# Performance work log

Measured on AMD Instinct MI355X. Metric: run time of the kernel, lower is better.

## Reference

```python
import jax, jax.numpy as jnp
import numpy as np

HIDDEN = 1024
HEADS = 16
HEAD_DIM = HIDDEN // HEADS  # 64
MAX_SEQ = 2048


def _rope_tables():
    # RotaryEmbedding buffers: freqs_cos/sin of shape [max_seq_len, head_dim//2]
    inv_freq = 1.0 / (10000.0 ** (jnp.arange(0, HEAD_DIM, 2, dtype=jnp.float32) / HEAD_DIM))
    t = jnp.arange(MAX_SEQ, dtype=jnp.float32)
    freqs = t[:, None] * inv_freq[None, :]
    return jnp.cos(freqs), jnp.sin(freqs)


def setup_inputs() -> dict:
    key = jax.random.key(0)
    k1, k2, k3 = jax.random.split(key, 3)
    x = jax.random.normal(k1, (2, 2048, HIDDEN), dtype=jnp.float32)
    qkv_w = jax.random.normal(k2, (HIDDEN, 3 * HIDDEN), dtype=jnp.float32) * 0.02
    qkv_b = jnp.zeros((3 * HIDDEN,), dtype=jnp.float32)
    out_w = jax.random.normal(k3, (HIDDEN, HIDDEN), dtype=jnp.float32) * 0.02
    out_b = jnp.zeros((HIDDEN,), dtype=jnp.float32)
    return {"x": x, "qkv_w": qkv_w, "qkv_b": qkv_b, "out_w": out_w, "out_b": out_b}


def reference(x, qkv_w, qkv_b, out_w, out_b):
    b, s, _ = x.shape
    qkv = x @ qkv_w + qkv_b                                   # [b, s, 3*hidden]
    qkv = qkv.reshape(b, s, HEADS, 3 * HEAD_DIM).transpose(0, 2, 1, 3)  # [b, h, s, 3*hd]
    q, k, v = jnp.split(qkv, 3, axis=-1)                      # each [b, h, s, hd]

    # Faithful to source quirk: rotary() is called on [b, h, s, hd] tensors so
    # x.shape[1] == num_heads -> seq_pos = arange(num_heads); tables are indexed
    # by HEAD index and broadcast over the sequence axis.
    cos_tab, sin_tab = _rope_tables()
    cos = cos_tab[:HEADS][None, :, None, :]                   # [1, h, 1, hd/2]
    sin = sin_tab[:HEADS][None, :, None, :]

    def rot(u):
        u1 = u[..., : HEAD_DIM // 2]
        u2 = u[..., HEAD_DIM // 2 :]
        return jnp.concatenate([u1 * cos - u2 * sin, u2 * cos + u1 * sin], axis=-1)

    q = rot(q)
    k = rot(k)

    scores = jnp.einsum("bhqd,bhkd->bhqk", q, k) / (HEAD_DIM ** 0.5)  # [b, h, s, s]
    attn = jax.nn.softmax(scores.astype(jnp.float32), axis=-1).astype(scores.dtype)
    out = jnp.einsum("bhqk,bhkd->bhqd", attn, v)              # [b, h, s, hd]
    out = out.transpose(0, 2, 1, 3).reshape(b, s, HEADS * HEAD_DIM)
    return out @ out_w + out_b
```

## Files before the change

### kernel.cpp

```cpp
#include <hip/hip_runtime.h>
#include <hip/hip_bf16.h>
#include <cstdint>
#include <cstddef>

typedef float  f32x4  __attribute__((ext_vector_type(4)));
typedef __bf16 bf16x8 __attribute__((ext_vector_type(8)));
typedef __bf16 bf16x4 __attribute__((ext_vector_type(4)));

#define HIDDEN 1024
#define SEQ    2048
#define BATCH  2
#define NQKV   3072
#define MTOT   4096

__device__ __forceinline__ __bf16 f2bf(float f) {
  unsigned u = __builtin_bit_cast(unsigned, f);
  u += 0x7FFFu + ((u >> 16) & 1u);
  unsigned short s = (unsigned short)(u >> 16);
  return __builtin_bit_cast(__bf16, s);
}

__device__ __forceinline__ unsigned pk2(float a, float b) {
  unsigned ua = __builtin_bit_cast(unsigned, a) + 0x8000u;
  unsigned ub = __builtin_bit_cast(unsigned, b) + 0x8000u;
  return __builtin_amdgcn_perm(ub, ua, 0x07060302u);
}

__device__ __forceinline__ float fexp2(float x) {
#if __has_builtin(__builtin_amdgcn_exp2f)
  return __builtin_amdgcn_exp2f(x);
#else
  return exp2f(x);
#endif
}

__device__ __forceinline__ void async16(const void* g, void* l) {
  __builtin_amdgcn_global_load_lds((__attribute__((address_space(1))) void*)(g),
                                   (__attribute__((address_space(3))) void*)(l),
                                   16, 0, 0);
}

#define MFMA16(a, b, c) __builtin_amdgcn_mfma_f32_16x16x32_bf16((a), (b), (c), 0, 0, 0)

__global__ __launch_bounds__(256) void k_prep(const float* __restrict__ x,
                                              __bf16* __restrict__ xb,
                                              const float* __restrict__ qkv_w,
                                              __bf16* __restrict__ wqkT,
                                              const float* __restrict__ out_w,
                                              __bf16* __restrict__ woT) {
  __shared__ float tile[64][65];
  const int bid = blockIdx.x, t = threadIdx.x;
  if (bid < 4096) {
    int i = bid * 256 + t;
    float4 v = ((const float4*)x)[i];
    bf16x4 o;
    o[0] = f2bf(v.x); o[1] = f2bf(v.y); o[2] = f2bf(v.z); o[3] = f2bf(v.w);
    ((bf16x4*)xb)[i] = o;
    return;
  }
  const float* W; __bf16* WT; int N, bx, by;
  if (bid < 4864) { int g = bid - 4096; W = qkv_w; WT = wqkT; N = NQKV;  bx = g % 48; by = g / 48; }
  else            { int g = bid - 4864; W = out_w; WT = woT;  N = HIDDEN; bx = g % 16; by = g / 16; }
  const int K = HIDDEN;
  int tx = t & 63, ty = t >> 6;
  int n0 = bx * 64, k0 = by * 64;
#pragma unroll
  for (int r = 0; r < 16; r++) {
    int row = r * 4 + ty;
    tile[row][tx] = W[(size_t)(k0 + row) * N + n0 + tx];
  }
  __syncthreads();
#pragma unroll
  for (int i2 = 0; i2 < 2; i2++) {
    int cc = i2 * 256 + t;
    int n = cc >> 3, ch = cc & 7;
    bf16x8 o;
#pragma unroll
    for (int j = 0; j < 8; j++) o[j] = f2bf(tile[ch * 8 + j][n]);
    *(bf16x8*)(WT + (size_t)(n0 + n) * K + k0 + ch * 8) = o;
  }
}

__global__ __launch_bounds__(512, 2) void k_qkv(const __bf16* __restrict__ A,
                                                const __bf16* __restrict__ BT,
                                                const float* __restrict__ bias,
                                                __bf16* __restrict__ Cout,
                                                __bf16* __restrict__ vt) {
  const int K = HIDDEN;
  __shared__ __align__(16) __bf16 As[2][2][8192];
  __shared__ __align__(16) __bf16 Bs[2][12288];
  const int t = threadIdx.x;
  const int lane = t & 63, wv = t >> 6;
  const int ln = lane & 15, quad = lane >> 4;
  const int wm = (wv >> 2) * 128, wn = (wv & 3) * 48;

  const int lin = blockIdx.x;
  const int xcd = lin & 7, wi = lin >> 3;
  const int bxi = (xcd & 3) * 4 + (wi & 3);
  const int byi = (xcd >> 2) * 8 + (wi >> 2);
  const int m0 = byi * 256, n0 = bxi * 192;

  auto stA = [&](int kt, int h) {
    __bf16* dst = &As[kt & 1][h][0];
    const __bf16* src = A + (size_t)m0 * K + kt * 64;
#pragma unroll
    for (int i = 0; i < 2; i++) {
      int tt = i * 512 + t;
      int sr = tt >> 3, ch = tt & 7;
      int gr = (sr & 63) + ((sr >> 6) << 7) + h * 64;
      async16(src + (size_t)gr * K + ((ch ^ (sr & 7)) * 8), dst + tt * 8);
    }
  };
  auto stB = [&](int kt) {
    __bf16* dst = &Bs[kt & 1][0];
    const __bf16* src = BT + (size_t)n0 * K + kt * 64;
#pragma unroll
    for (int i = 0; i < 3; i++) {
      int tt = i * 512 + t;
      int row = tt >> 3, ch = tt & 7;
      async16(src + (size_t)row * K + ((ch ^ (row & 7)) * 8), dst + tt * 8);
    }
  };

  const f32x4 zero4 = {0.f, 0.f, 0.f, 0.f};
  f32x4 acc[8][3];
#pragma unroll
  for (int i = 0; i < 8; i++)
#pragma unroll
    for (int j = 0; j < 3; j++) acc[i][j] = zero4;

  stA(0, 0); stB(0); stA(0, 1); stA(1, 0); stB(1);

  bf16x8 a0[4], a1[4], b0[3], b1[3];
  const int sra = ln + ((wv >> 2) << 6);
  const int srb = (wv & 3) * 48 + ln;
  const int swz = ln & 7;

  const int NT = K / 64;
  for (int kt = 0; kt < NT; kt++) {
    const int p = kt & 1;
    if (kt < NT - 1) asm volatile("s_waitcnt vmcnt(5)" ::: "memory");
    else             asm volatile("s_waitcnt vmcnt(0)" ::: "memory");
    __builtin_amdgcn_s_barrier();
    const __bf16* A0 = &As[p][0][0];
    const __bf16* A1 = &As[p][1][0];
    const __bf16* Bb = &Bs[p][0];
    {
#pragma unroll
      for (int m = 0; m < 4; m++)
        a0[m] = *(const bf16x8*)(A0 + (sra + m * 16) * 64 + ((quad ^ swz) * 8));
#pragma unroll
      for (int n = 0; n < 3; n++)
        b0[n] = *(const bf16x8*)(Bb + (srb + n * 16) * 64 + ((quad ^ swz) * 8));
      if (kt + 1 < NT) stA(kt + 1, 1);
      __builtin_amdgcn_s_barrier();
      asm volatile("s_waitcnt lgkmcnt(0)" ::: "memory");
      __builtin_amdgcn_sched_barrier(0);
      __builtin_amdgcn_s_setprio(1);
#pragma unroll
      for (int m = 0; m < 4; m++)
#pragma unroll
        for (int n = 0; n < 3; n++)
          acc[m][n] = MFMA16(a0[m], b0[n], acc[m][n]);
      __builtin_amdgcn_s_setprio(0);
      __builtin_amdgcn_s_barrier();
    }
    {
#pragma unroll
      for (int m = 0; m < 4; m++)
        a1[m] = *(const bf16x8*)(A0 + (sra + m * 16) * 64 + (((4 + quad) ^ swz) * 8));
#pragma unroll
      for (int n = 0; n < 3; n++)
        b1[n] = *(const bf16x8*)(Bb + (srb + n * 16) * 64 + (((4 + quad) ^ swz) * 8));
      __builtin_amdgcn_s_barrier();
      asm volatile("s_waitcnt lgkmcnt(0)" ::: "memory");
      __builtin_amdgcn_sched_barrier(0);
      __builtin_amdgcn_s_setprio(1);
#pragma unroll
      for (int m = 0; m < 4; m++)
#pragma unroll
        for (int n = 0; n < 3; n++)
          acc[m][n] = MFMA16(a1[m], b1[n], acc[m][n]);
      __builtin_amdgcn_s_setprio(0);
      __builtin_amdgcn_s_barrier();
    }
    {
#pragma unroll
      for (int m = 0; m < 4; m++)
        a0[m] = *(const bf16x8*)(A1 + (sra + m * 16) * 64 + ((quad ^ swz) * 8));
      if (kt + 2 < NT) stA(kt + 2, 0);
      __builtin_amdgcn_s_barrier();
      asm volatile("s_waitcnt lgkmcnt(0)" ::: "memory");
      __builtin_amdgcn_sched_barrier(0);
      __builtin_amdgcn_s_setprio(1);
#pragma unroll
      for (int m = 0; m < 4; m++)
#pragma unroll
        for (int n = 0; n < 3; n++)
          acc[4 + m][n] = MFMA16(a0[m], b0[n], acc[4 + m][n]);
      __builtin_amdgcn_s_setprio(0);
      __builtin_amdgcn_s_barrier();
    }
    {
#pragma unroll
      for (int m = 0; m < 4; m++)
        a1[m] = *(const bf16x8*)(A1 + (sra + m * 16) * 64 + (((4 + quad) ^ swz) * 8));
      if (kt + 2 < NT) stB(kt + 2);
      __builtin_amdgcn_s_barrier();
      asm volatile("s_waitcnt lgkmcnt(0)" ::: "memory");
      __builtin_amdgcn_sched_barrier(0);
      __builtin_amdgcn_s_setprio(1);
#pragma unroll
      for (int m = 0; m < 4; m++)
#pragma unroll
        for (int n = 0; n < 3; n++)
          acc[4 + m][n] = MFMA16(a1[m], b1[n], acc[4 + m][n]);
      __builtin_amdgcn_s_setprio(0);
    }
  }

  const float CE = 0.125f * 1.44269504089f;
#pragma unroll
  for (int nt = 0; nt < 3; nt++) {
    int g = n0 + wn + nt * 16;
    int col = g + ln;
    float bv = bias[col];
    int off = g % 192;
    if (off < 128) {
      float scl = (off < 64) ? CE : 1.0f;
#pragma unroll
      for (int mt = 0; mt < 8; mt++) {
#pragma unroll
        for (int r = 0; r < 4; r++) {
          int row = m0 + wm + mt * 16 + quad * 4 + r;
          Cout[(size_t)row * NQKV + col] = f2bf((acc[mt][nt][r] + bv) * scl);
        }
      }
    } else {
      int hg = g / 192;
      int d  = off - 128 + ln;
#pragma unroll
      for (int mt = 0; mt < 8; mt++) {
        int rowb = m0 + wm + mt * 16;
        int bb = rowb >> 11;
        int s  = rowb & 2047;
        int sblk = s >> 7;
        int blk  = (s >> 4) & 7;
        int pp = (blk & 3) * 32 + quad * 8 + ((blk >> 2) << 2);
        uint2 o;
        o.x = pk2(acc[mt][nt][0] + bv, acc[mt][nt][1] + bv);
        o.y = pk2(acc[mt][nt][2] + bv, acc[mt][nt][3] + bv);
        *(uint2*)(vt + ((size_t)((bb * 16 + hg) * 64 + d)) * SEQ + sblk * 128 + pp) = o;
      }
    }
  }
}

__global__ __launch_bounds__(256, 4) void k_gemm_out(const __bf16* __restrict__ A,
                                                     const __bf16* __restrict__ BT,
                                                     const float* __restrict__ bias,
                                                     float* __restrict__ Cout,
                                                     int M, int N, int K) {
  constexpr int TN = 64;
  __shared__ __align__(16) __bf16 As[2 * 128 * 32];
  __shared__ __align__(16) __bf16 Bs[2 * TN * 32];
  const int t = threadIdx.x;
  const int lane = t & 63, wv = t >> 6;
  const int ln = lane & 15, quad = lane >> 4;
  const int sw8 = (quad ^ ((ln >> 1) & 3)) * 8;
  const int wm = (wv & 1) * 64, wn = (wv >> 1) * (TN / 2);

  const int nbx = N / TN;
  const int cx = nbx >> 1;
  const int lin = blockIdx.x;
  const int xcd = lin & 7, wi = lin >> 3;
  const int bxi = (xcd & 1) * cx + wi % cx;
  const int byi = (xcd >> 1) * 8 + wi / cx;
  const int m0 = byi * 128, n0 = bxi * TN;

  auto stage = [&](int k0, int p) {
    __bf16* Ad = As + p * (128 * 32);
    __bf16* Bd = Bs + p * (TN * 32);
#pragma unroll
    for (int i = 0; i < 2; i++) {
      int tt = i * 256 + t;
      int row = tt >> 2, ch = tt & 3;
      int chs = ch ^ ((row >> 1) & 3);
      async16(A + (size_t)(m0 + row) * K + k0 + chs * 8, Ad + tt * 8);
    }
    {
      int tt = t;
      int row = tt >> 2, ch = tt & 3;
      int chs = ch ^ ((row >> 1) & 3);
      async16(BT + (size_t)(n0 + row) * K + k0 + chs * 8, Bd + tt * 8);
    }
  };

  const f32x4 zero4 = {0.f, 0.f, 0.f, 0.f};
  f32x4 acc[4][2];
#pragma unroll
  for (int i = 0; i < 4; i++)
#pragma unroll
    for (int j = 0; j < 2; j++) acc[i][j] = zero4;

  stage(0, 0);
  const int NIT = K / 32;
  for (int it = 0; it < NIT; it++) {
    __syncthreads();
    if (it + 1 < NIT) stage((it + 1) * 32, (it + 1) & 1);
    const __bf16* Asb = As + (it & 1) * (128 * 32);
    const __bf16* Bsb = Bs + (it & 1) * (TN * 32);
    bf16x8 af[4], bfr[2];
#pragma unroll
    for (int x = 0; x < 4; x++)
      af[x] = *(const bf16x8*)(Asb + (wm + x * 16 + ln) * 32 + sw8);
#pragma unroll
    for (int x = 0; x < 2; x++)
      bfr[x] = *(const bf16x8*)(Bsb + (wn + x * 16 + ln) * 32 + sw8);
#pragma unroll
    for (int mt = 0; mt < 4; mt++)
#pragma unroll
      for (int nt = 0; nt < 2; nt++)
        acc[mt][nt] = MFMA16(af[mt], bfr[nt], acc[mt][nt]);
  }
#pragma unroll
  for (int nt = 0; nt < 2; nt++) {
    int col = n0 + wn + nt * 16 + ln;
    float bv = bias[col];
#pragma unroll
    for (int mt = 0; mt < 4; mt++) {
#pragma unroll
      for (int r = 0; r < 4; r++) {
        int row = m0 + wm + mt * 16 + quad * 4 + r;
        Cout[(size_t)row * N + col] = acc[mt][nt][r] + bv;
      }
    }
  }
}

__global__ __launch_bounds__(512, 4) void k_attn(const __bf16* __restrict__ qkv,
                                                 const __bf16* __restrict__ vt,
                                                 __bf16* __restrict__ aout) {
  __shared__ __align__(16) __bf16 smem[32768];
  const int t = threadIdx.x;
  const int lane = t & 63, wv = t >> 6;
  const int ln = lane & 15, quad = lane >> 4;
  const int sw8 = (quad ^ ((ln >> 1) & 3)) * 8;

  int gid = blockIdx.x;
  int slot = gid & 7, j = gid >> 3;
  int bh = slot * 4 + (j >> 4);
  int qt0 = j & 15;
  const int b = bh >> 4, h = bh & 15;
  const int q0 = qt0 * 128;

  const __bf16* qbase = qkv + (size_t)b * SEQ * NQKV + h * 192;
  const __bf16* kbase = qbase + 64;
  const __bf16* vbase = vt + (size_t)bh * 64 * SEQ;

#pragma unroll
  for (int i = 0; i < 2; i++) {
    int tt = i * 512 + t;
    int hh = tt >> 9, row = (tt >> 2) & 127, ch = tt & 3;
    int chs = ch ^ ((row >> 1) & 3);
    async16(kbase + (size_t)row * NQKV + hh * 32 + chs * 8, smem + tt * 8);
  }
#pragma unroll
  for (int i = 0; i < 2; i++) {
    int tt = i * 512 + t;
    int c = tt >> 8, d = (tt >> 2) & 63, w = tt & 3;
    int ws = w ^ ((d >> 1) & 3);
    async16(vbase + (size_t)d * SEQ + c * 32 + ws * 8, smem + 16384 + tt * 8);
  }

  bf16x8 qf[2];
#pragma unroll
  for (int dc = 0; dc < 2; dc++)
    qf[dc] = *(const bf16x8*)(qbase + (size_t)(q0 + wv * 16 + ln) * NQKV + dc * 32 + quad * 8);

  union { unsigned u[4]; bf16x8 v; } ones;
  ones.u[0] = ones.u[1] = ones.u[2] = ones.u[3] = 0x3F803F80u;

  const f32x4 zero4 = {0.f, 0.f, 0.f, 0.f};
  f32x4 O[4];
  f32x4 Ol = zero4;
#pragma unroll
  for (int dt = 0; dt < 4; dt++) O[dt] = zero4;

  for (int it = 0; it < SEQ / 128; it++) {
    __syncthreads();
    const __bf16* Ks = smem + (it & 1) * 8192;
    const __bf16* Vs = smem + 16384 + (it & 1) * 8192;
    if (it + 1 < SEQ / 128) {
      __bf16* Kd = smem + ((it + 1) & 1) * 8192;
      __bf16* Vd = smem + 16384 + ((it + 1) & 1) * 8192;
      const __bf16* kn = kbase + (size_t)(it + 1) * 128 * NQKV;
      const __bf16* vn = vbase + (it + 1) * 128;
#pragma unroll
      for (int i = 0; i < 2; i++) {
        int tt = i * 512 + t;
        int hh = tt >> 9, row = (tt >> 2) & 127, ch = tt & 3;
        int chs = ch ^ ((row >> 1) & 3);
        async16(kn + (size_t)row * NQKV + hh * 32 + chs * 8, Kd + tt * 8);
      }
#pragma unroll
      for (int i = 0; i < 2; i++) {
        int tt = i * 512 + t;
        int c = tt >> 8, d = (tt >> 2) & 63, w = tt & 3;
        int ws = w ^ ((d >> 1) & 3);
        async16(vn + (size_t)d * SEQ + c * 32 + ws * 8, Vd + tt * 8);
      }
    }

    unsigned Pp[8][2];
#pragma unroll
    for (int blk = 0; blk < 8; blk++) {
      bf16x8 kf0 = *(const bf16x8*)(Ks +        (blk * 16 + ln) * 32 + sw8);
      bf16x8 kf1 = *(const bf16x8*)(Ks + 4096 + (blk * 16 + ln) * 32 + sw8);
      __builtin_amdgcn_s_setprio(1);
      f32x4 s = MFMA16(kf0, qf[0], zero4);
      s = MFMA16(kf1, qf[1], s);
      __builtin_amdgcn_s_setprio(0);
      Pp[blk][0] = pk2(fexp2(s[0]), fexp2(s[1]));
      Pp[blk][1] = pk2(fexp2(s[2]), fexp2(s[3]));
    }
#pragma unroll
    for (int kc = 0; kc < 4; kc++) {
      union { bf16x8 v; unsigned u[4]; } pf;
      pf.u[0] = Pp[kc][0]; pf.u[1] = Pp[kc][1];
      pf.u[2] = Pp[kc + 4][0]; pf.u[3] = Pp[kc + 4][1];
      __builtin_amdgcn_s_setprio(1);
      Ol = MFMA16(pf.v, ones.v, Ol);
#pragma unroll
      for (int dt = 0; dt < 4; dt++) {
        bf16x8 vf = *(const bf16x8*)(Vs + kc * 2048 + (dt * 16 + ln) * 32 + sw8);
        O[dt] = MFMA16(pf.v, vf, O[dt]);
      }
      __builtin_amdgcn_s_setprio(0);
    }
  }

  __bf16* stage = smem + wv * 1024;
#pragma unroll
  for (int r = 0; r < 4; r++) {
    float ir = 1.0f / Ol[r];
#pragma unroll
    for (int dt = 0; dt < 4; dt++)
      stage[(quad * 4 + r) * 64 + dt * 16 + ln] = f2bf(O[dt][r] * ir);
  }
  __bf16* obase = aout + (size_t)(b * SEQ + q0 + wv * 16) * HIDDEN + h * 64;
#pragma unroll
  for (int i = 0; i < 2; i++) {
    int tt = i * 64 + lane; int row = tt >> 3, ch = tt & 7;
    *(bf16x8*)(obase + (size_t)row * HIDDEN + ch * 8) = *(const bf16x8*)(stage + row * 64 + ch * 8);
  }
}

extern "C" void kernel_launch(void* const* d_in, const int* in_sizes, int n_in,
                              void* d_out, int out_size, void* d_ws, size_t ws_size,
                              hipStream_t stream) {
  const float* x     = (const float*)d_in[0];
  const float* qkv_w = (const float*)d_in[1];
  const float* qkv_b = (const float*)d_in[2];
  const float* out_w = (const float*)d_in[3];
  const float* out_b = (const float*)d_in[4];

  char* ws = (char*)d_ws;
  __bf16* xb   = (__bf16*)(ws);
  __bf16* wqkT = (__bf16*)(ws + 8388608);
  __bf16* woT  = (__bf16*)(ws + 14680064);
  __bf16* qkv  = (__bf16*)(ws + 16777216);
  __bf16* vt   = (__bf16*)(ws + 41943040);
  __bf16* aout = (__bf16*)(ws + 50331648);

  k_prep<<<5120, 256, 0, stream>>>(x, xb, qkv_w, wqkT, out_w, woT);
  k_qkv<<<256, 512, 0, stream>>>(xb, wqkT, qkv_b, qkv, vt);
  k_attn<<<512, 512, 0, stream>>>(qkv, vt, aout);
  k_gemm_out<<<512, 256, 0, stream>>>(aout, woT, out_b, (float*)d_out, MTOT, HIDDEN, HIDDEN);
}
```

Before: 177.4 us.

## Rewrite output projection GEMM with 128x128 tiles and split-half async pipeline

Replaces the 128x64-tile, 256-thread output GEMM with a 128x128-tile, 512-thread kernel that uses K-steps of 64. Each A tile is split into two halves with staggered async loads, manual vmcnt/lgkmcnt waits, explicit barriers and raised wave priority around the MFMA blocks. The aim is to raise data reuse per loaded byte and to overlap global loads with MFMA work. In exchange it launches half as many blocks and adds more barriers per iteration. This GEMM is only a small part of the total runtime.

```diff
diff --git a/kernel.cpp b/kernel.cpp
--- a/kernel.cpp
+++ b/kernel.cpp
@@ -256,43 +256,39 @@
   }
 }
 
-__global__ __launch_bounds__(256, 4) void k_gemm_out(const __bf16* __restrict__ A,
-                                                     const __bf16* __restrict__ BT,
-                                                     const float* __restrict__ bias,
-                                                     float* __restrict__ Cout,
-                                                     int M, int N, int K) {
-  constexpr int TN = 64;
-  __shared__ __align__(16) __bf16 As[2 * 128 * 32];
-  __shared__ __align__(16) __bf16 Bs[2 * TN * 32];
+__global__ __launch_bounds__(512, 2) void k_out(const __bf16* __restrict__ A,
+                                                const __bf16* __restrict__ BT,
+                                                const float* __restrict__ bias,
+                                                float* __restrict__ Cout) {
+  const int K = HIDDEN, N = HIDDEN;
+  __shared__ __align__(16) __bf16 As[2][2][4096];
+  __shared__ __align__(16) __bf16 Bs[2][8192];
   const int t = threadIdx.x;
   const int lane = t & 63, wv = t >> 6;
   const int ln = lane & 15, quad = lane >> 4;
-  const int sw8 = (quad ^ ((ln >> 1) & 3)) * 8;
-  const int wm = (wv & 1) * 64, wn = (wv >> 1) * (TN / 2);
-
-  const int nbx = N / TN;
-  const int cx = nbx >> 1;
+  const int wm = (wv >> 2) * 64, wn = (wv & 3) * 32;
+
   const int lin = blockIdx.x;
   const int xcd = lin & 7, wi = lin >> 3;
-  const int bxi = (xcd & 1) * cx + wi % cx;
-  const int byi = (xcd >> 1) * 8 + wi / cx;
-  const int m0 = byi * 128, n0 = bxi * TN;
-
-  auto stage = [&](int k0, int p) {
-    __bf16* Ad = As + p * (128 * 32);
-    __bf16* Bd = Bs + p * (TN * 32);
+  const int bxi = (xcd & 1) * 4 + (wi & 3);
+  const int byi = (xcd >> 1) * 8 + (wi >> 2);
+  const int m0 = byi * 128, n0 = bxi * 128;
+
+  auto stA = [&](int kt, int h) {
+    __bf16* dst = &As[kt & 1][h][0];
+    const __bf16* src = A + (size_t)m0 * K + kt * 64;
+    int sr = t >> 3, ch = t & 7;
+    int gr = (sr & 31) + ((sr >> 5) << 6) + h * 32;
+    async16(src + (size_t)gr * K + ((ch ^ (sr & 7)) * 8), dst + t * 8);
+  };
+  auto stB = [&](int kt) {
+    __bf16* dst = &Bs[kt & 1][0];
+    const __bf16* src = BT + (size_t)n0 * K + kt * 64;
 #pragma unroll
     for (int i = 0; i < 2; i++) {
-      int tt = i * 256 + t;
-      int row = tt >> 2, ch = tt & 3;
-      int chs = ch ^ ((row >> 1) & 3);
-      async16(A + (size_t)(m0 + row) * K + k0 + chs * 8, Ad + tt * 8);
-    }
-    {
-      int tt = t;
-      int row = tt >> 2, ch = tt & 3;
-      int chs = ch ^ ((row >> 1) & 3);
-      async16(BT + (size_t)(n0 + row) * K + k0 + chs * 8, Bd + tt * 8);
+      int tt = i * 512 + t;
+      int row = tt >> 3, ch = tt & 7;
+      async16(src + (size_t)row * K + ((ch ^ (row & 7)) * 8), dst + tt * 8);
     }
   };
 
@@ -303,39 +299,84 @@
 #pragma unroll
     for (int j = 0; j < 2; j++) acc[i][j] = zero4;
 
-  stage(0, 0);
-  const int NIT = K / 32;
-  for (int it = 0; it < NIT; it++) {
-    __syncthreads();
-    if (it + 1 < NIT) stage((it + 1) * 32, (it + 1) & 1);
-    const __bf16* Asb = As + (it & 1) * (128 * 32);
-    const __bf16* Bsb = Bs + (it & 1) * (TN * 32);
-    bf16x8 af[4], bfr[2];
-#pragma unroll
-    for (int x = 0; x < 4; x++)
-      af[x] = *(const bf16x8*)(Asb + (wm + x * 16 + ln) * 32 + sw8);
-#pragma unroll
-    for (int x = 0; x < 2; x++)
-      bfr[x] = *(const bf16x8*)(Bsb + (wn + x * 16 + ln) * 32 + sw8);
-#pragma unroll
-    for (int mt = 0; mt < 4; mt++)
-#pragma unroll
-      for (int nt = 0; nt < 2; nt++)
-        acc[mt][nt] = MFMA16(af[mt], bfr[nt], acc[mt][nt]);
-  }
-#pragma unroll
-  for (int nt = 0; nt < 2; nt++) {
-    int col = n0 + wn + nt * 16 + ln;
-    float bv = bias[col];
-#pragma unroll
-    for (int mt = 0; mt < 4; mt++) {
-#pragma unroll
-      for (int r = 0; r < 4; r++) {
-        int row = m0 + wm + mt * 16 + quad * 4 + r;
-        Cout[(size_t)row * N + col] = acc[mt][nt][r] + bv;
-      }
-    }
-  }
+  stA(0, 0); stB(0); stA(0, 1); stA(1, 0); stB(1);
+
+  bf16x8 af[2][2], bfr[2][2];
+  const int sra = ln + ((wv >> 2) << 5);
+  const int srb = wn + ln;
+  const int swz = ln & 7;
+
+  const int NT = K / 64;
+  for (int kt = 0; kt < NT; kt++) {
+    const int p = kt & 1;
+    if (kt < NT - 1) asm volatile("s_waitcnt vmcnt(3)" ::: "memory");
+    else             asm volatile("s_waitcnt vmcnt(0)" ::: "memory");
+    __builtin_amdgcn_s_barrier();
+    const __bf16* A0 = &As[p][0][0];
+    const __bf16* A1 = &As[p][1][0];
+    const __bf16* Bb = &Bs[p][0];
+    {
+#pragma unroll
+      for (int m = 0; m < 2; m++)
+#pragma unroll
+        for (int kk = 0; kk < 2; kk++)
+          af[m][kk] = *(const bf16x8*)(A0 + (sra + m * 16) * 64 + (((kk * 4 + quad) ^ swz) * 8));
+#pragma unroll
+      for (int n = 0; n < 2; n++)
+#pragma unroll
+        for (int kk = 0; kk < 2; kk++)
+          bfr[n][kk] = *(const bf16x8*)(Bb + (srb + n * 16) * 64 + (((kk * 4 + quad) ^ swz) * 8));
+      if (kt + 1 < NT) stA(kt + 1, 1);
+      __builtin_amdgcn_s_barrier();
+      asm volatile("s_waitcnt lgkmcnt(0)" ::: "memory");
+      __builtin_amdgcn_sched_barrier(0);
+      __builtin_amdgcn_s_setprio(1);
+#pragma unroll
+      for (int m = 0; m < 2; m++)
+#pragma unroll
+        for (int n = 0; n < 2; n++) {
+          acc[m][n] = MFMA16(af[m][0], bfr[n][0], acc[m][n]);
+          acc[m][n] = MFMA16(af[m][1], bfr[n][1], acc[m][n]);
+        }
+      __builtin_amdgcn_s_setprio(0);
+      __builtin_amdgcn_s_barrier();
+    }
+    {
+#pragma unroll
+      for (int m = 0; m < 2; m++)
+#pragma unroll
+        for (int kk = 0; kk < 2; kk++)
+          af[m][kk] = *(const bf16x8*)(A1 + (sra + m * 16) * 64 + (((kk * 4 + quad) ^ swz) * 8));
+      if (kt + 2 < NT) { stA(kt + 2, 0); stB(kt + 2); }
+      __builtin_amdgcn_s_barrier();
+      asm volatile("s_waitcnt lgkmcnt(0)" ::: "memory");
+      __builtin_amdgcn_sched_barrier(0);
+      __builtin_amdgcn_s_setprio(1);
+#pragma unroll
+      for (int m = 0; m < 2; m++)
+#pragma unroll
+        for (int n = 0; n < 2; n++) {
+          acc[2 + m][n] = MFMA16(af[m][0], bfr[n][0], acc[2 + m][n]);
+          acc[2 + m][n] = MFMA16(af[m][1], bfr[n][1], acc[2 + m][n]);
+        }
+      __builtin_amdgcn_s_setprio(0);
+    }
+  }
+
+#pragma unroll
+  for (int h = 0; h < 2; h++)
+#pragma unroll
+    for (int n = 0; n < 2; n++) {
+      int col = n0 + wn + n * 16 + ln;
+      float bv = bias[col];
+#pragma unroll
+      for (int m = 0; m < 2; m++)
+#pragma unroll
+        for (int r = 0; r < 4; r++) {
+          int row = m0 + wm + h * 32 + m * 16 + quad * 4 + r;
+          Cout[(size_t)row * N + col] = acc[h * 2 + m][n][r] + bv;
+        }
+    }
 }
 
 __global__ __launch_bounds__(512, 4) void k_attn(const __bf16* __restrict__ qkv,
@@ -476,5 +517,5 @@
   k_prep<<<5120, 256, 0, stream>>>(x, xb, qkv_w, wqkT, out_w, woT);
   k_qkv<<<256, 512, 0, stream>>>(xb, wqkT, qkv_b, qkv, vt);
   k_attn<<<512, 512, 0, stream>>>(qkv, vt, aout);
-  k_gemm_out<<<512, 256, 0, stream>>>(aout, woT, out_b, (float*)d_out, MTOT, HIDDEN, HIDDEN);
-}
+  k_out<<<256, 512, 0, stream>>>(aout, woT, out_b, (float*)d_out);
+}
```

Result: faster. 172.4 us (median of 3 runs) (-2.9%).
